# Performance work log

Hardware: AMD Instinct MI355X
Metric: run time of the kernel (lower is better)

Reference implementation:

```python
import jax, jax.numpy as jnp
import numpy as np

EMBED = 128
NUM_HOPS = 3
VOCAB = 32000
MEM = 50
PAD = 0


def pos_weights(J, d):
    # MemN2N position encoding: 1 - (j+1)/J - (k+1)/d * (1 - 2*(j+1)/J)
    j = jnp.arange(J, dtype=jnp.float32)[:, None]
    k = jnp.arange(d, dtype=jnp.float32)[None, :]
    return 1.0 - (j + 1.0) / J - (k + 1.0) / d * (1.0 - 2.0 * (j + 1.0) / J)


def setup_inputs() -> dict:
    key = jax.random.key(0)
    ks = jax.random.split(key, 10)
    ctx_query = jax.random.randint(ks[0], (16, 10, 20), 0, VOCAB)
    story = jax.random.randint(ks[1], (16, MEM, 40), 0, VOCAB)

    def emb(k):
        w = 0.1 * jax.random.normal(k, (VOCAB, EMBED), dtype=jnp.float32)
        return w.at[PAD].set(0.0)  # padding_idx row is zero

    A_w = emb(ks[2])
    C_w = emb(ks[3])
    B_w = emb(ks[4])
    H_w = 0.1 * jax.random.normal(ks[5], (EMBED, EMBED), dtype=jnp.float32)
    H_b = 0.1 * jax.random.normal(ks[6], (EMBED,), dtype=jnp.float32)
    out_w = 0.1 * jax.random.normal(ks[7], (VOCAB, EMBED), dtype=jnp.float32)
    TA = 0.1 * jax.random.normal(ks[8], (MEM, EMBED), dtype=jnp.float32)
    TC = 0.1 * jax.random.normal(ks[9], (MEM, EMBED), dtype=jnp.float32)
    return {"ctx_query": ctx_query, "story": story, "A_w": A_w, "C_w": C_w,
            "B_w": B_w, "H_w": H_w, "H_b": H_b, "out_w": out_w, "TA": TA, "TC": TC}


def reference(ctx_query, story, A_w, C_w, B_w, H_w, H_b, out_w, TA, TC):
    B, NQ, S = ctx_query.shape
    R, S2 = story.shape[1], story.shape[2]
    cq = ctx_query.reshape(B * NQ, S)
    # story repeated across num_qa (broadcast instead of materialized repeat)
    st = jnp.broadcast_to(story[:, None], (B, NQ, R, S2)).reshape(B * NQ, R, S2)

    qw = pos_weights(S, EMBED)            # [S, d]
    state = jnp.sum(B_w[cq] * qw, axis=1)  # [BN, d]

    sw = pos_weights(S2, EMBED)           # [S2, d]
    for _ in range(NUM_HOPS):             # use_lw=True: A/C tied across hops
        mem = jnp.sum(A_w[st] * sw, axis=2) + TA    # [BN, R, d]
        outm = jnp.sum(C_w[st] * sw, axis=2) + TC   # [BN, R, d]
        probs = jax.nn.softmax(jnp.einsum('brd,bd->br', mem, state), axis=-1)
        response = jnp.einsum('br,brd->bd', probs, outm)  # [BN, d]
        state = response @ H_w.T + H_b + state      # H(response) + state
    return state @ out_w.T                          # [BN, vocab]
```

## Files before the change

### kernel.cpp

```cpp
#include <hip/hip_runtime.h>
#include <hip/hip_bf16.h>
#include <math.h>

#define EMBED 128
#define VOCAB 32000
#define MEMN  50
#define BATCH 16
#define NQ    10
#define SQ    20
#define SS    40
#define BN    (BATCH*NQ)
#define NHOPS 3
#define NV    64

typedef short v8s __attribute__((ext_vector_type(8)));
typedef float v4f __attribute__((ext_vector_type(4)));

#define MFMA16 __builtin_amdgcn_mfma_f32_16x16x32_bf16

__device__ __forceinline__ float posw(int j, int J, int k) {
    float jf = (float)(j + 1) / (float)J;
    return 1.0f - jf - ((float)(k + 1) / (float)EMBED) * (1.0f - 2.0f * jf);
}

__device__ __forceinline__ short f2bf(float f) {
    __hip_bfloat16 h = __float2bfloat16(f);
    return *(short*)&h;
}

__global__ void k_embed(const int* __restrict__ cq, const int* __restrict__ story,
                        const float* __restrict__ Bw, const float* __restrict__ Aw,
                        const float* __restrict__ Cw, const float* __restrict__ TA,
                        const float* __restrict__ TC,
                        float* __restrict__ state, float* __restrict__ memb,
                        float* __restrict__ outb) {
    int blk = blockIdx.x;
    int t = threadIdx.x;
    if (blk < BN) {
        float acc = 0.f;
        #pragma unroll
        for (int s = 0; s < SQ; ++s) {
            int tok = cq[blk * SQ + s];
            acc += Bw[tok * EMBED + t] * posw(s, SQ, t);
        }
        state[blk * EMBED + t] = acc;
    } else {
        int br = blk - BN;
        int r = br % MEMN;
        float ma = TA[r * EMBED + t];
        float mc = TC[r * EMBED + t];
        const int* toks = story + br * SS;
        #pragma unroll 4
        for (int s = 0; s < SS; ++s) {
            int tok = toks[s];
            float w = posw(s, SS, t);
            ma += Aw[tok * EMBED + t] * w;
            mc += Cw[tok * EMBED + t] * w;
        }
        memb[br * EMBED + t] = ma;
        outb[br * EMBED + t] = mc;
    }
}

__global__ __launch_bounds__(512) void k_hops(const float* __restrict__ memb,
                                              const float* __restrict__ outb,
                                              const float* __restrict__ Hw,
                                              const float* __restrict__ Hb,
                                              const float* __restrict__ state,
                                              __hip_bfloat16* __restrict__ stateb) {
    __shared__ float lmem[MEMN][EMBED + 1];
    __shared__ float lout[MEMN][EMBED + 1];
    __shared__ float lstate[EMBED];
    __shared__ float lpart[8][52];
    __shared__ float lprobs[52];
    __shared__ float lrespp[4][EMBED];
    __shared__ float lHp[4][EMBED];

    int bn = blockIdx.x;
    int b  = bn / NQ;
    int t  = threadIdx.x;
    int w  = t >> 6;
    int l  = t & 63;
    int d  = t & 127;
    int g  = t >> 7;

    {
        const float4* mb4 = (const float4*)(memb + (size_t)b * MEMN * EMBED);
        const float4* ob4 = (const float4*)(outb + (size_t)b * MEMN * EMBED);
        for (int i = t; i < MEMN * EMBED / 4; i += 512) {
            int r = i >> 5, c = (i & 31) << 2;
            float4 v = mb4[i];
            lmem[r][c] = v.x; lmem[r][c+1] = v.y; lmem[r][c+2] = v.z; lmem[r][c+3] = v.w;
            float4 u = ob4[i];
            lout[r][c] = u.x; lout[r][c+1] = u.y; lout[r][c+2] = u.z; lout[r][c+3] = u.w;
        }
        if (t < EMBED) lstate[t] = state[bn * EMBED + t];
    }
    float hbd = (t < EMBED) ? Hb[t] : 0.f;
    __syncthreads();

    for (int hop = 0; hop < NHOPS; ++hop) {
        if (l < MEMN) {
            int d0 = w << 4;
            float a0 = 0.f, a1 = 0.f, a2 = 0.f, a3 = 0.f;
            #pragma unroll
            for (int j = 0; j < 16; j += 4) {
                a0 += lmem[l][d0 + j]     * lstate[d0 + j];
                a1 += lmem[l][d0 + j + 1] * lstate[d0 + j + 1];
                a2 += lmem[l][d0 + j + 2] * lstate[d0 + j + 2];
                a3 += lmem[l][d0 + j + 3] * lstate[d0 + j + 3];
            }
            lpart[w][l] = (a0 + a1) + (a2 + a3);
        }
        __syncthreads();
        if (t < 64) {
            float lg = -1e30f;
            if (t < MEMN) {
                float s0 = (lpart[0][t] + lpart[1][t]) + (lpart[2][t] + lpart[3][t]);
                float s1 = (lpart[4][t] + lpart[5][t]) + (lpart[6][t] + lpart[7][t]);
                lg = s0 + s1;
            }
            float mx = lg;
            #pragma unroll
            for (int off = 32; off; off >>= 1) mx = fmaxf(mx, __shfl_xor(mx, off, 64));
            float e = (t < MEMN) ? __expf(lg - mx) : 0.f;
            float ss = e;
            #pragma unroll
            for (int off = 32; off; off >>= 1) ss += __shfl_xor(ss, off, 64);
            if (t < MEMN) lprobs[t] = e / ss;
        }
        __syncthreads();
        {
            float r0 = 0.f, r1 = 0.f;
            #pragma unroll
            for (int k = 0; k + 4 < MEMN; k += 8) {
                int ra = g + k, rb = g + k + 4;
                r0 += lprobs[ra] * lout[ra][d];
                r1 += lprobs[rb] * lout[rb][d];
            }
            if (g < 2) { int ra = g + 48; r0 += lprobs[ra] * lout[ra][d]; }
            lrespp[g][d] = r0 + r1;
        }
        __syncthreads();
        {
            int ks = g << 5;
            const float4* hw4 = (const float4*)&Hw[(size_t)d * EMBED + ks];
            float a0 = 0.f, a1 = 0.f, a2 = 0.f, a3 = 0.f;
            #pragma unroll
            for (int j = 0; j < 8; ++j) {
                float4 wv = hw4[j];
                int k = ks + (j << 2);
                float v0 = (lrespp[0][k]     + lrespp[1][k])     + (lrespp[2][k]     + lrespp[3][k]);
                float v1 = (lrespp[0][k + 1] + lrespp[1][k + 1]) + (lrespp[2][k + 1] + lrespp[3][k + 1]);
                float v2 = (lrespp[0][k + 2] + lrespp[1][k + 2]) + (lrespp[2][k + 2] + lrespp[3][k + 2]);
                float v3 = (lrespp[0][k + 3] + lrespp[1][k + 3]) + (lrespp[2][k + 3] + lrespp[3][k + 3]);
                a0 += v0 * wv.x; a1 += v1 * wv.y; a2 += v2 * wv.z; a3 += v3 * wv.w;
            }
            lHp[g][d] = (a0 + a1) + (a2 + a3);
        }
        __syncthreads();
        if (t < EMBED) {
            float ns = hbd + lstate[t]
                     + (lHp[0][t] + lHp[1][t]) + (lHp[2][t] + lHp[3][t]);
            lstate[t] = ns;
        }
        __syncthreads();
    }
    if (t < EMBED)
        stateb[bn * EMBED + t] = __float2bfloat16(lstate[t]);
}

__global__ __launch_bounds__(256) void k_out(const __hip_bfloat16* __restrict__ stateb,
                                             const float* __restrict__ outw,
                                             float* __restrict__ out) {
    __shared__ __align__(16) __hip_bfloat16 Alds[BN][EMBED + 8];
    __shared__ __align__(16) __hip_bfloat16 Blds[NV][EMBED + 8];
    int t = threadIdx.x;
    int vbase = blockIdx.x * NV;

    #pragma unroll
    for (int i = 0; i < 10; ++i) {
        int e = t + i * 256;
        int row = e >> 4, c8 = (e & 15) << 3;
        *(int4*)&Alds[row][c8] = *(const int4*)&stateb[row * EMBED + c8];
    }
    #pragma unroll
    for (int i = 0; i < 8; ++i) {
        int e = t + i * 256;
        int row = e >> 5, c4 = (e & 31) << 2;
        float4 w = *(const float4*)&outw[(size_t)(vbase + row) * EMBED + c4];
        short4 p;
        p.x = f2bf(w.x); p.y = f2bf(w.y); p.z = f2bf(w.z); p.w = f2bf(w.w);
        *(short4*)&Blds[row][c4] = p;
    }
    __syncthreads();

    int wv = t >> 6;
    int l = t & 63;
    int col16 = l & 15;
    int kg = l >> 4;

    v8s bfrag[4];
    #pragma unroll
    for (int k4 = 0; k4 < 4; ++k4)
        bfrag[k4] = *(v8s*)&Blds[(wv << 4) + col16][k4 * 32 + kg * 8];

    v4f acc[10];
    #pragma unroll
    for (int m = 0; m < 10; ++m) acc[m] = (v4f){0.f, 0.f, 0.f, 0.f};

    #pragma unroll
    for (int k4 = 0; k4 < 4; ++k4) {
        #pragma unroll
        for (int m = 0; m < 10; ++m) {
            v8s af = *(v8s*)&Alds[m * 16 + col16][k4 * 32 + kg * 8];
            acc[m] = MFMA16(af, bfrag[k4], acc[m], 0, 0, 0);
        }
    }

    int colg = vbase + (wv << 4) + col16;
    #pragma unroll
    for (int m = 0; m < 10; ++m) {
        #pragma unroll
        for (int i = 0; i < 4; ++i) {
            out[(size_t)(m * 16 + kg * 4 + i) * VOCAB + colg] = acc[m][i];
        }
    }
}

extern "C" void kernel_launch(void* const* d_in, const int* in_sizes, int n_in,
                              void* d_out, int out_size, void* d_ws, size_t ws_size,
                              hipStream_t stream) {
    const int*   ctx_query = (const int*)  d_in[0];
    const int*   story     = (const int*)  d_in[1];
    const float* A_w       = (const float*)d_in[2];
    const float* C_w       = (const float*)d_in[3];
    const float* B_w       = (const float*)d_in[4];
    const float* H_w       = (const float*)d_in[5];
    const float* H_b       = (const float*)d_in[6];
    const float* out_w     = (const float*)d_in[7];
    const float* TA        = (const float*)d_in[8];
    const float* TC        = (const float*)d_in[9];
    float* out = (float*)d_out;

    float* ws    = (float*)d_ws;
    float* state = ws;
    float* memb  = state + BN * EMBED;
    float* outb  = memb + BATCH * MEMN * EMBED;
    __hip_bfloat16* stateb = (__hip_bfloat16*)(outb + BATCH * MEMN * EMBED);

    k_embed<<<BN + BATCH * MEMN, 128, 0, stream>>>(
        ctx_query, story, B_w, A_w, C_w, TA, TC, state, memb, outb);
    k_hops<<<BN, 512, 0, stream>>>(memb, outb, H_w, H_b, state, stateb);
    k_out<<<VOCAB / NV, 256, 0, stream>>>(stateb, out_w, out);
}
```

Before: 29.78 us.

## Precompute H·outm per memory slot and fold query embedding into hop kernel

Uses linearity to push the H matrix multiply through the probability-weighted sum: each story memory row of C embeddings is pre-multiplied by H_w once in the embedding kernel, so each hop only needs a weighted sum over 50 precomputed rows. The A and C embeddings are split into separate blocks to expose more parallelism, and the query embedding moves into the hop kernel, which drops the separate state buffer. This removes two barriers and the per-hop H matvec from the serial hop loop. In exchange the embedding kernel does extra matvec work, and the hop weighted sum now runs on only 128 of 512 threads.

```diff
diff --git a/kernel.cpp b/kernel.cpp
--- a/kernel.cpp
+++ b/kernel.cpp
@@ -12,6 +12,7 @@
 #define BN    (BATCH*NQ)
 #define NHOPS 3
 #define NV    64
+#define NST   (BATCH*MEMN)
 
 typedef short v8s __attribute__((ext_vector_type(8)));
 typedef float v4f __attribute__((ext_vector_type(4)));
@@ -28,53 +29,64 @@
     return *(short*)&h;
 }
 
-__global__ void k_embed(const int* __restrict__ cq, const int* __restrict__ story,
-                        const float* __restrict__ Bw, const float* __restrict__ Aw,
-                        const float* __restrict__ Cw, const float* __restrict__ TA,
-                        const float* __restrict__ TC,
-                        float* __restrict__ state, float* __restrict__ memb,
-                        float* __restrict__ outb) {
+__global__ void k_embed(const int* __restrict__ story,
+                        const float* __restrict__ Aw, const float* __restrict__ Cw,
+                        const float* __restrict__ TA, const float* __restrict__ TC,
+                        const float* __restrict__ Hw,
+                        float* __restrict__ memb, float* __restrict__ OHm) {
+    __shared__ float lrow[EMBED];
     int blk = blockIdx.x;
     int t = threadIdx.x;
-    if (blk < BN) {
-        float acc = 0.f;
-        #pragma unroll
-        for (int s = 0; s < SQ; ++s) {
-            int tok = cq[blk * SQ + s];
-            acc += Bw[tok * EMBED + t] * posw(s, SQ, t);
-        }
-        state[blk * EMBED + t] = acc;
-    } else {
-        int br = blk - BN;
+    if (blk < NST) {
+        int br = blk;
         int r = br % MEMN;
         float ma = TA[r * EMBED + t];
+        const int* toks = story + br * SS;
+        #pragma unroll 4
+        for (int s = 0; s < SS; ++s) {
+            int tok = toks[s];
+            ma += Aw[tok * EMBED + t] * posw(s, SS, t);
+        }
+        memb[br * EMBED + t] = ma;
+    } else {
+        int br = blk - NST;
+        int r = br % MEMN;
         float mc = TC[r * EMBED + t];
         const int* toks = story + br * SS;
         #pragma unroll 4
         for (int s = 0; s < SS; ++s) {
             int tok = toks[s];
-            float w = posw(s, SS, t);
-            ma += Aw[tok * EMBED + t] * w;
-            mc += Cw[tok * EMBED + t] * w;
-        }
-        memb[br * EMBED + t] = ma;
-        outb[br * EMBED + t] = mc;
-    }
-}
-
-__global__ __launch_bounds__(512) void k_hops(const float* __restrict__ memb,
-                                              const float* __restrict__ outb,
-                                              const float* __restrict__ Hw,
+            mc += Cw[tok * EMBED + t] * posw(s, SS, t);
+        }
+        lrow[t] = mc;
+        __syncthreads();
+        const float4* hw4 = (const float4*)&Hw[(size_t)t * EMBED];
+        float a0 = 0.f, a1 = 0.f, a2 = 0.f, a3 = 0.f;
+        #pragma unroll 8
+        for (int j = 0; j < 32; ++j) {
+            float4 wv = hw4[j];
+            int k = j << 2;
+            a0 += lrow[k]     * wv.x;
+            a1 += lrow[k + 1] * wv.y;
+            a2 += lrow[k + 2] * wv.z;
+            a3 += lrow[k + 3] * wv.w;
+        }
+        OHm[br * EMBED + t] = (a0 + a1) + (a2 + a3);
+    }
+}
+
+__global__ __launch_bounds__(512) void k_hops(const int* __restrict__ cq,
+                                              const float* __restrict__ Bw,
+                                              const float* __restrict__ memb,
+                                              const float* __restrict__ OHm,
                                               const float* __restrict__ Hb,
-                                              const float* __restrict__ state,
                                               __hip_bfloat16* __restrict__ stateb) {
     __shared__ float lmem[MEMN][EMBED + 1];
-    __shared__ float lout[MEMN][EMBED + 1];
+    __shared__ float lOH[MEMN][EMBED + 1];
     __shared__ float lstate[EMBED];
+    __shared__ float lqp[4][EMBED];
     __shared__ float lpart[8][52];
     __shared__ float lprobs[52];
-    __shared__ float lrespp[4][EMBED];
-    __shared__ float lHp[4][EMBED];
 
     int bn = blockIdx.x;
     int b  = bn / NQ;
@@ -82,21 +94,32 @@
     int w  = t >> 6;
     int l  = t & 63;
     int d  = t & 127;
-    int g  = t >> 7;
+    int sg = t >> 7;
 
     {
         const float4* mb4 = (const float4*)(memb + (size_t)b * MEMN * EMBED);
-        const float4* ob4 = (const float4*)(outb + (size_t)b * MEMN * EMBED);
+        const float4* oh4 = (const float4*)(OHm  + (size_t)b * MEMN * EMBED);
         for (int i = t; i < MEMN * EMBED / 4; i += 512) {
             int r = i >> 5, c = (i & 31) << 2;
             float4 v = mb4[i];
             lmem[r][c] = v.x; lmem[r][c+1] = v.y; lmem[r][c+2] = v.z; lmem[r][c+3] = v.w;
-            float4 u = ob4[i];
-            lout[r][c] = u.x; lout[r][c+1] = u.y; lout[r][c+2] = u.z; lout[r][c+3] = u.w;
-        }
-        if (t < EMBED) lstate[t] = state[bn * EMBED + t];
+            float4 u = oh4[i];
+            lOH[r][c] = u.x; lOH[r][c+1] = u.y; lOH[r][c+2] = u.z; lOH[r][c+3] = u.w;
+        }
+        const int* toks = cq + bn * SQ;
+        float acc = 0.f;
+        #pragma unroll
+        for (int i = 0; i < SQ / 4; ++i) {
+            int s = sg + (i << 2);
+            int tok = toks[s];
+            acc += Bw[(size_t)tok * EMBED + d] * posw(s, SQ, d);
+        }
+        lqp[sg][d] = acc;
     }
     float hbd = (t < EMBED) ? Hb[t] : 0.f;
+    __syncthreads();
+    if (t < EMBED)
+        lstate[t] = (lqp[0][t] + lqp[1][t]) + (lqp[2][t] + lqp[3][t]);
     __syncthreads();
 
     for (int hop = 0; hop < NHOPS; ++hop) {
@@ -130,39 +153,18 @@
             if (t < MEMN) lprobs[t] = e / ss;
         }
         __syncthreads();
-        {
-            float r0 = 0.f, r1 = 0.f;
-            #pragma unroll
-            for (int k = 0; k + 4 < MEMN; k += 8) {
-                int ra = g + k, rb = g + k + 4;
-                r0 += lprobs[ra] * lout[ra][d];
-                r1 += lprobs[rb] * lout[rb][d];
+        if (t < EMBED) {
+            float a0 = 0.f, a1 = 0.f, a2 = 0.f, a3 = 0.f;
+            #pragma unroll
+            for (int r = 0; r < 48; r += 4) {
+                a0 += lprobs[r]     * lOH[r][t];
+                a1 += lprobs[r + 1] * lOH[r + 1][t];
+                a2 += lprobs[r + 2] * lOH[r + 2][t];
+                a3 += lprobs[r + 3] * lOH[r + 3][t];
             }
-            if (g < 2) { int ra = g + 48; r0 += lprobs[ra] * lout[ra][d]; }
-            lrespp[g][d] = r0 + r1;
-        }
-        __syncthreads();
-        {
-            int ks = g << 5;
-            const float4* hw4 = (const float4*)&Hw[(size_t)d * EMBED + ks];
-            float a0 = 0.f, a1 = 0.f, a2 = 0.f, a3 = 0.f;
-            #pragma unroll
-            for (int j = 0; j < 8; ++j) {
-                float4 wv = hw4[j];
-                int k = ks + (j << 2);
-                float v0 = (lrespp[0][k]     + lrespp[1][k])     + (lrespp[2][k]     + lrespp[3][k]);
-                float v1 = (lrespp[0][k + 1] + lrespp[1][k + 1]) + (lrespp[2][k + 1] + lrespp[3][k + 1]);
-                float v2 = (lrespp[0][k + 2] + lrespp[1][k + 2]) + (lrespp[2][k + 2] + lrespp[3][k + 2]);
-                float v3 = (lrespp[0][k + 3] + lrespp[1][k + 3]) + (lrespp[2][k + 3] + lrespp[3][k + 3]);
-                a0 += v0 * wv.x; a1 += v1 * wv.y; a2 += v2 * wv.z; a3 += v3 * wv.w;
-            }
-            lHp[g][d] = (a0 + a1) + (a2 + a3);
-        }
-        __syncthreads();
-        if (t < EMBED) {
-            float ns = hbd + lstate[t]
-                     + (lHp[0][t] + lHp[1][t]) + (lHp[2][t] + lHp[3][t]);
-            lstate[t] = ns;
+            a0 += lprobs[48] * lOH[48][t];
+            a1 += lprobs[49] * lOH[49][t];
+            lstate[t] = hbd + lstate[t] + (a0 + a1) + (a2 + a3);
         }
         __syncthreads();
     }
@@ -243,14 +245,14 @@
     const float* TC        = (const float*)d_in[9];
     float* out = (float*)d_out;
 
-    float* ws    = (float*)d_ws;
-    float* state = ws;
-    float* memb  = state + BN * EMBED;
-    float* outb  = memb + BATCH * MEMN * EMBED;
-    __hip_bfloat16* stateb = (__hip_bfloat16*)(outb + BATCH * MEMN * EMBED);
-
-    k_embed<<<BN + BATCH * MEMN, 128, 0, stream>>>(
-        ctx_query, story, B_w, A_w, C_w, TA, TC, state, memb, outb);
-    k_hops<<<BN, 512, 0, stream>>>(memb, outb, H_w, H_b, state, stateb);
+    float* ws   = (float*)d_ws;
+    float* memb = ws;
+    float* OHm  = memb + NST * EMBED;
+    __hip_bfloat16* stateb = (__hip_bfloat16*)(OHm + NST * EMBED);
+
+    k_embed<<<NST * 2, 128, 0, stream>>>(
+        story, A_w, C_w, TA, TC, H_w, memb, OHm);
+    k_hops<<<BN, 512, 0, stream>>>(
+        ctx_query, B_w, memb, OHm, H_b, stateb);
     k_out<<<VOCAB / NV, 256, 0, stream>>>(stateb, out_w, out);
 }
```

New measurement: 34.67 us. 16.4% more time.

## Fuse embed, hops and output GEMM into one cooperative kernel

Applied to the files above, without the earlier changes.

Replaces the three separate launches with one cooperative kernel of 512 blocks that uses grid-wide syncs between the embedding, hop and output-projection phases. Blocks with no hop work prefetch and convert their out_w tile to bf16 in LDS during the hop phase, so part of the output GEMM's load overlaps the serial hop computation. The aim is to remove launch gaps and hide memory latency. In exchange it pays for two grid barriers and an occupancy query on every call, and falls back to the old three-kernel path if the cooperative launch is not possible.

```diff
diff --git a/kernel.cpp b/kernel.cpp
--- a/kernel.cpp
+++ b/kernel.cpp
@@ -1,6 +1,9 @@
 #include <hip/hip_runtime.h>
 #include <hip/hip_bf16.h>
+#include <hip/hip_cooperative_groups.h>
 #include <math.h>
+
+namespace cg = cooperative_groups;
 
 #define EMBED 128
 #define VOCAB 32000
@@ -12,6 +15,9 @@
 #define BN    (BATCH*NQ)
 #define NHOPS 3
 #define NV    64
+#define NST   (BATCH*MEMN)
+#define NOUT  (VOCAB/NV)
+#define MGRID 512
 
 typedef short v8s __attribute__((ext_vector_type(8)));
 typedef float v4f __attribute__((ext_vector_type(4)));
@@ -26,6 +32,225 @@
 __device__ __forceinline__ short f2bf(float f) {
     __hip_bfloat16 h = __float2bfloat16(f);
     return *(short*)&h;
+}
+
+union __align__(16) Smem {
+    struct {
+        float lmem[MEMN][EMBED + 1];
+        float lout[MEMN][EMBED + 1];
+        float lstate[EMBED];
+        float lpart[4][52];
+        float lprobs[52];
+        float lrespp[2][EMBED];
+        float lHp[2][EMBED];
+    } h;
+    struct {
+        short Alds[BN][EMBED + 8];
+        short Blds[NV][EMBED + 8];
+    } o;
+};
+
+__global__ __launch_bounds__(256) void mega(
+    const int* __restrict__ cq, const int* __restrict__ story,
+    const float* __restrict__ Bw, const float* __restrict__ Aw,
+    const float* __restrict__ Cw, const float* __restrict__ TA,
+    const float* __restrict__ TC, const float* __restrict__ Hw,
+    const float* __restrict__ Hb, const float* __restrict__ outw,
+    float* __restrict__ state, float* __restrict__ memb,
+    float* __restrict__ outb, __hip_bfloat16* __restrict__ stateb,
+    float* __restrict__ out)
+{
+    __shared__ Smem sm;
+    cg::grid_group grid = cg::this_grid();
+    int blk = blockIdx.x;
+    int t = threadIdx.x;
+
+    {
+        int half = t >> 7, th = t & 127;
+        int item = blk * 2 + half;
+        if (item < BN) {
+            float acc = 0.f;
+            const int* toks = cq + item * SQ;
+            #pragma unroll
+            for (int s = 0; s < SQ; ++s) {
+                int tok = toks[s];
+                acc += Bw[tok * EMBED + th] * posw(s, SQ, th);
+            }
+            state[item * EMBED + th] = acc;
+        } else if (item < BN + NST) {
+            int br = item - BN;
+            int r = br % MEMN;
+            float ma = TA[r * EMBED + th];
+            float mc = TC[r * EMBED + th];
+            const int* toks = story + br * SS;
+            #pragma unroll 4
+            for (int s = 0; s < SS; ++s) {
+                int tok = toks[s];
+                float w = posw(s, SS, th);
+                ma += Aw[tok * EMBED + th] * w;
+                mc += Cw[tok * EMBED + th] * w;
+            }
+            memb[br * EMBED + th] = ma;
+            outb[br * EMBED + th] = mc;
+        }
+    }
+    grid.sync();
+
+    if (blk < BN) {
+        int bn = blk;
+        int b  = bn / NQ;
+        int w  = t >> 6;
+        int l  = t & 63;
+        int d  = t & 127;
+        int h  = t >> 7;
+
+        {
+            const float4* mb4 = (const float4*)(memb + (size_t)b * MEMN * EMBED);
+            const float4* ob4 = (const float4*)(outb + (size_t)b * MEMN * EMBED);
+            for (int i = t; i < MEMN * EMBED / 4; i += 256) {
+                int r = i >> 5, c = (i & 31) << 2;
+                float4 v = mb4[i];
+                sm.h.lmem[r][c] = v.x; sm.h.lmem[r][c+1] = v.y;
+                sm.h.lmem[r][c+2] = v.z; sm.h.lmem[r][c+3] = v.w;
+                float4 u = ob4[i];
+                sm.h.lout[r][c] = u.x; sm.h.lout[r][c+1] = u.y;
+                sm.h.lout[r][c+2] = u.z; sm.h.lout[r][c+3] = u.w;
+            }
+            if (t < EMBED) sm.h.lstate[t] = state[bn * EMBED + t];
+        }
+        float hbd = (t < EMBED) ? Hb[t] : 0.f;
+        __syncthreads();
+
+        for (int hop = 0; hop < NHOPS; ++hop) {
+            if (l < MEMN) {
+                int d0 = w << 5;
+                float a0 = 0.f, a1 = 0.f, a2 = 0.f, a3 = 0.f;
+                #pragma unroll
+                for (int j = 0; j < 32; j += 4) {
+                    a0 += sm.h.lmem[l][d0 + j]     * sm.h.lstate[d0 + j];
+                    a1 += sm.h.lmem[l][d0 + j + 1] * sm.h.lstate[d0 + j + 1];
+                    a2 += sm.h.lmem[l][d0 + j + 2] * sm.h.lstate[d0 + j + 2];
+                    a3 += sm.h.lmem[l][d0 + j + 3] * sm.h.lstate[d0 + j + 3];
+                }
+                sm.h.lpart[w][l] = (a0 + a1) + (a2 + a3);
+            }
+            __syncthreads();
+            if (t < 64) {
+                float lg = (t < MEMN)
+                    ? (sm.h.lpart[0][t] + sm.h.lpart[1][t]) +
+                      (sm.h.lpart[2][t] + sm.h.lpart[3][t]) : -1e30f;
+                float mx = lg;
+                #pragma unroll
+                for (int off = 32; off; off >>= 1) mx = fmaxf(mx, __shfl_xor(mx, off, 64));
+                float e = (t < MEMN) ? __expf(lg - mx) : 0.f;
+                float ss = e;
+                #pragma unroll
+                for (int off = 32; off; off >>= 1) ss += __shfl_xor(ss, off, 64);
+                if (t < MEMN) sm.h.lprobs[t] = e / ss;
+            }
+            __syncthreads();
+            {
+                float r0 = 0.f, r1 = 0.f;
+                int k0 = h * 25;
+                #pragma unroll
+                for (int k = 0; k < 24; k += 2) {
+                    r0 += sm.h.lprobs[k0 + k]     * sm.h.lout[k0 + k][d];
+                    r1 += sm.h.lprobs[k0 + k + 1] * sm.h.lout[k0 + k + 1][d];
+                }
+                r0 += sm.h.lprobs[k0 + 24] * sm.h.lout[k0 + 24][d];
+                sm.h.lrespp[h][d] = r0 + r1;
+            }
+            __syncthreads();
+            {
+                int ks = h << 6;
+                const float4* hw4 = (const float4*)&Hw[(size_t)d * EMBED + ks];
+                float a0 = 0.f, a1 = 0.f, a2 = 0.f, a3 = 0.f;
+                #pragma unroll
+                for (int j = 0; j < 16; ++j) {
+                    float4 wv = hw4[j];
+                    int k = ks + (j << 2);
+                    a0 += (sm.h.lrespp[0][k]     + sm.h.lrespp[1][k])     * wv.x;
+                    a1 += (sm.h.lrespp[0][k + 1] + sm.h.lrespp[1][k + 1]) * wv.y;
+                    a2 += (sm.h.lrespp[0][k + 2] + sm.h.lrespp[1][k + 2]) * wv.z;
+                    a3 += (sm.h.lrespp[0][k + 3] + sm.h.lrespp[1][k + 3]) * wv.w;
+                }
+                sm.h.lHp[h][d] = (a0 + a1) + (a2 + a3);
+            }
+            __syncthreads();
+            if (t < EMBED) {
+                float ns = hbd + sm.h.lstate[t] + sm.h.lHp[0][t] + sm.h.lHp[1][t];
+                sm.h.lstate[t] = ns;
+            }
+            __syncthreads();
+        }
+        if (t < EMBED)
+            stateb[bn * EMBED + t] = __float2bfloat16(sm.h.lstate[t]);
+    } else if (blk < NOUT) {
+        int vbase = blk * NV;
+        #pragma unroll
+        for (int i = 0; i < 8; ++i) {
+            int e = t + i * 256;
+            int row = e >> 5, c4 = (e & 31) << 2;
+            float4 w = *(const float4*)&outw[(size_t)(vbase + row) * EMBED + c4];
+            short4 p;
+            p.x = f2bf(w.x); p.y = f2bf(w.y); p.z = f2bf(w.z); p.w = f2bf(w.w);
+            *(short4*)&sm.o.Blds[row][c4] = p;
+        }
+    }
+    grid.sync();
+
+    if (blk < NOUT) {
+        int vbase = blk * NV;
+        if (blk < BN) {
+            #pragma unroll
+            for (int i = 0; i < 8; ++i) {
+                int e = t + i * 256;
+                int row = e >> 5, c4 = (e & 31) << 2;
+                float4 w = *(const float4*)&outw[(size_t)(vbase + row) * EMBED + c4];
+                short4 p;
+                p.x = f2bf(w.x); p.y = f2bf(w.y); p.z = f2bf(w.z); p.w = f2bf(w.w);
+                *(short4*)&sm.o.Blds[row][c4] = p;
+            }
+        }
+        #pragma unroll
+        for (int i = 0; i < 10; ++i) {
+            int e = t + i * 256;
+            int row = e >> 4, c8 = (e & 15) << 3;
+            *(int4*)&sm.o.Alds[row][c8] = *(const int4*)&stateb[row * EMBED + c8];
+        }
+        __syncthreads();
+
+        int wv = t >> 6;
+        int l = t & 63;
+        int col16 = l & 15;
+        int kg = l >> 4;
+
+        v8s bfrag[4];
+        #pragma unroll
+        for (int k4 = 0; k4 < 4; ++k4)
+            bfrag[k4] = *(v8s*)&sm.o.Blds[(wv << 4) + col16][k4 * 32 + kg * 8];
+
+        v4f acc[10];
+        #pragma unroll
+        for (int m = 0; m < 10; ++m) acc[m] = (v4f){0.f, 0.f, 0.f, 0.f};
+
+        #pragma unroll
+        for (int k4 = 0; k4 < 4; ++k4) {
+            #pragma unroll
+            for (int m = 0; m < 10; ++m) {
+                v8s af = *(v8s*)&sm.o.Alds[m * 16 + col16][k4 * 32 + kg * 8];
+                acc[m] = MFMA16(af, bfrag[k4], acc[m], 0, 0, 0);
+            }
+        }
+
+        int colg = vbase + (wv << 4) + col16;
+        #pragma unroll
+        for (int m = 0; m < 10; ++m) {
+            #pragma unroll
+            for (int i = 0; i < 4; ++i)
+                out[(size_t)(m * 16 + kg * 4 + i) * VOCAB + colg] = acc[m][i];
+        }
+    }
 }
 
 __global__ void k_embed(const int* __restrict__ cq, const int* __restrict__ story,
@@ -246,11 +471,26 @@
     float* ws    = (float*)d_ws;
     float* state = ws;
     float* memb  = state + BN * EMBED;
-    float* outb  = memb + BATCH * MEMN * EMBED;
-    __hip_bfloat16* stateb = (__hip_bfloat16*)(outb + BATCH * MEMN * EMBED);
-
-    k_embed<<<BN + BATCH * MEMN, 128, 0, stream>>>(
-        ctx_query, story, B_w, A_w, C_w, TA, TC, state, memb, outb);
-    k_hops<<<BN, 512, 0, stream>>>(memb, outb, H_w, H_b, state, stateb);
-    k_out<<<VOCAB / NV, 256, 0, stream>>>(stateb, out_w, out);
-}
+    float* outb  = memb + NST * EMBED;
+    __hip_bfloat16* stateb = (__hip_bfloat16*)(outb + NST * EMBED);
+
+    int maxB = 0;
+    bool coop = (hipOccupancyMaxActiveBlocksPerMultiprocessor(&maxB, mega, 256, 0)
+                 == hipSuccess) && (maxB >= 2);
+    if (coop) {
+        void* args[] = {
+            (void*)&ctx_query, (void*)&story, (void*)&B_w, (void*)&A_w, (void*)&C_w,
+            (void*)&TA, (void*)&TC, (void*)&H_w, (void*)&H_b, (void*)&out_w,
+            (void*)&state, (void*)&memb, (void*)&outb, (void*)&stateb, (void*)&out
+        };
+        hipError_t rc = hipLaunchCooperativeKernel((const void*)mega, dim3(MGRID),
+                                                   dim3(256), args, 0, stream);
+        if (rc != hipSuccess) { (void)hipGetLastError(); coop = false; }
+    }
+    if (!coop) {
+        k_embed<<<BN + NST, 128, 0, stream>>>(
+            ctx_query, story, B_w, A_w, C_w, TA, TC, state, memb, outb);
+        k_hops<<<BN, 512, 0, stream>>>(memb, outb, H_w, H_b, state, stateb);
+        k_out<<<VOCAB / NV, 256, 0, stream>>>(stateb, out_w, out);
+    }
+}
```

Result: no change. 29.82 us (+0.1%).
